# Kernel tuning notes

Hardware: AMD Instinct MI355X
Metric: run time of the kernel (lower is better)

Reference implementation:

```python
import jax, jax.numpy as jnp
import numpy as np

B, S, C = 128, 512, 64
H, D = 4, 32  # num_heads, units


def setup_inputs() -> dict:
    key = jax.random.key(0)
    ks = jax.random.split(key, 6)
    scale_in = 1.0 / np.sqrt(C)
    scale_cat = 1.0 / np.sqrt(H * D)
    return {
        "inputs": jax.random.normal(ks[0], (B, S, C), dtype=jnp.float32),
        "Wq": jax.random.normal(ks[1], (H, C, D), dtype=jnp.float32) * scale_in,
        "bq": jnp.zeros((H, D), dtype=jnp.float32),
        "Wk": jax.random.normal(ks[2], (H, C, D), dtype=jnp.float32) * scale_in,
        "bk": jnp.zeros((H, D), dtype=jnp.float32),
        "Wv": jax.random.normal(ks[3], (H, C, D), dtype=jnp.float32) * scale_in,
        "bv": jnp.zeros((H, D), dtype=jnp.float32),
        "Wo": jax.random.normal(ks[4], (H * D, D), dtype=jnp.float32) * scale_cat,
        "bo": jnp.zeros((D,), dtype=jnp.float32),
    }


def reference(inputs, Wq, bq, Wk, bk, Wv, bv, Wo, bo):
    # Batched QKV projections over all heads at once (fuses the per-head loop).
    # inputs: [B,S,C]; Wq/Wk/Wv: [H,C,D]; biases: [H,D]
    Q = jnp.einsum("bsc,hcd->bhsd", inputs, Wq) + bq[None, :, None, :]
    K = jnp.einsum("bsc,hcd->bhsd", inputs, Wk) + bk[None, :, None, :]
    V = jnp.einsum("bsc,hcd->bhsd", inputs, Wv) + bv[None, :, None, :]
    scale = 1.0 / jnp.sqrt(jnp.asarray(D, dtype=inputs.dtype))
    scores = jnp.einsum("bhsd,bhtd->bhst", Q, K) * scale  # [B,H,S,S]
    attn = jax.nn.softmax(scores, axis=-1)
    ctx = jnp.einsum("bhst,bhtd->bhsd", attn, V)  # [B,H,S,D]
    # Concatenate heads along feature dim (head 0 first, matching tf.concat order)
    concat = jnp.transpose(ctx, (0, 2, 1, 3)).reshape(inputs.shape[0], inputs.shape[1], H * D)
    return concat @ Wo + bo
```

## Files before the change

kernel.cpp:

```cpp
#include <hip/hip_runtime.h>
#include <hip/hip_bf16.h>

#define B_ 128
#define S_ 512
#define C_ 64
#define H_ 4
#define D_ 32
#define QSCALE_LOG2E 0.25505654249765306f

typedef __attribute__((ext_vector_type(8))) short bf16x8;
typedef __attribute__((ext_vector_type(8))) unsigned short u16x8;
typedef __attribute__((ext_vector_type(4))) unsigned short u16x4;
typedef __attribute__((ext_vector_type(4))) float f32x4;
typedef __attribute__((ext_vector_type(4))) unsigned int u32x4;
typedef __attribute__((ext_vector_type(2))) unsigned int u32x2;

__device__ __forceinline__ unsigned short f2bf(float f) {
    unsigned int u = __float_as_uint(f);
    u = (u + 0x7FFFu + ((u >> 16) & 1u)) >> 16;
    return (unsigned short)u;
}
__device__ __forceinline__ unsigned int pk2(float a, float b) {
    __hip_bfloat162 h = __float22bfloat162_rn(float2{a, b});
    unsigned int r;
    __builtin_memcpy(&r, &h, sizeof(r));
    return r;
}

__global__ __launch_bounds__(256) void wprep_kernel(
    const float* __restrict__ Wq, const float* __restrict__ bq,
    const float* __restrict__ Wk, const float* __restrict__ bk,
    const float* __restrict__ Wv, const float* __restrict__ bv,
    unsigned short* __restrict__ Wt, float* __restrict__ bias)
{
    const int bid = blockIdx.x, tid = threadIdx.x;
    if (bid < 96) {
        const int idx = bid * 256 + tid;
        const int m = idx >> 13, f = idx & 8191;
        const int h = f >> 11, c = (f >> 5) & 63, d = f & 31;
        const float* W = (m == 0) ? Wq : (m == 1) ? Wk : Wv;
        float v = W[f] * ((m == 0) ? QSCALE_LOG2E : 1.0f);
        Wt[(size_t)(m * 128 + h * 32 + d) * 64 + c] = f2bf(v);
    } else {
        for (int idx = tid; idx < 384; idx += 256) {
            int m = idx >> 7, o = idx & 127;
            const float* bs = (m == 0) ? bq : (m == 1) ? bk : bv;
            bias[idx] = bs[o] * ((m == 0) ? QSCALE_LOG2E : 1.0f);
        }
    }
}

__global__ __launch_bounds__(256, 4) void qkv_kernel(
    const float* __restrict__ X, const unsigned short* __restrict__ Wt,
    const float* __restrict__ bias,
    unsigned short* __restrict__ Qo, unsigned short* __restrict__ Ko,
    unsigned short* __restrict__ Vo)
{
    __shared__ unsigned int Xs[128 * 36];

    const int tid  = threadIdx.x;
    const int row0 = blockIdx.x * 128;
    const int w    = tid >> 6, lane = tid & 63;
    const int lq   = lane & 15, lg = lane >> 4;

    {
        const float4* Xg = reinterpret_cast<const float4*>(X + (size_t)row0 * C_);
        #pragma unroll
        for (int k = 0; k < 8; ++k) {
            int f4 = tid + k * 256;
            int r = f4 >> 4, c4 = f4 & 15;
            float4 x = Xg[f4];
            u32x2 p;
            p[0] = pk2(x.x, x.y);
            p[1] = pk2(x.z, x.w);
            *reinterpret_cast<u32x2*>(&Xs[r * 36 + c4 * 2]) = p;
        }
    }
    __syncthreads();

    const int b  = row0 / S_;
    const int sb = row0 % S_;

    #pragma unroll
    for (int m = 0; m < 3; ++m) {
        const unsigned short* Wtm = Wt + (size_t)(m * 128) * 64;
        const float* bm = bias + m * 128;
        unsigned short* Out = (m == 0) ? Qo : (m == 1) ? Ko : Vo;

        #pragma unroll
        for (int ni = 0; ni < 2; ++ni) {
            const int nt = 2 * w + ni;
            const int n0 = nt * 16;
            bf16x8 wf0 = *reinterpret_cast<const bf16x8*>(Wtm + (size_t)(n0 + lq) * 64 + lg * 8);
            bf16x8 wf1 = *reinterpret_cast<const bf16x8*>(Wtm + (size_t)(n0 + lq) * 64 + 32 + lg * 8);

            if (m != 2) {
                const int nrow = n0 + 4 * lg;
                const int h = nrow >> 5, d0 = nrow & 31;
                f32x4 bv4 = *reinterpret_cast<const f32x4*>(bm + nrow);
                unsigned short* obase = Out + ((size_t)(b * H_ + h) * S_ + sb) * D_ + d0;
                #pragma unroll
                for (int st = 0; st < 8; ++st) {
                    const unsigned int* xr = &Xs[(st * 16 + lq) * 36];
                    bf16x8 xf0 = *reinterpret_cast<const bf16x8*>(xr + lg * 4);
                    bf16x8 xf1 = *reinterpret_cast<const bf16x8*>(xr + 16 + lg * 4);
                    f32x4 acc;
                    acc[0] = 0.f; acc[1] = 0.f; acc[2] = 0.f; acc[3] = 0.f;
                    acc = __builtin_amdgcn_mfma_f32_16x16x32_bf16(wf0, xf0, acc, 0, 0, 0);
                    acc = __builtin_amdgcn_mfma_f32_16x16x32_bf16(wf1, xf1, acc, 0, 0, 0);
                    u32x2 cc;
                    cc[0] = pk2(acc[0] + bv4[0], acc[1] + bv4[1]);
                    cc[1] = pk2(acc[2] + bv4[2], acc[3] + bv4[3]);
                    *reinterpret_cast<u32x2*>(obase + (size_t)(st * 16 + lq) * D_) = cc;
                }
            } else {
                const int ncol = n0 + lq;
                const int h = ncol >> 5, d = ncol & 31;
                const float bsc = bm[ncol];
                unsigned short* obase = Out + ((size_t)(b * H_ + h) * S_) * D_
                                      + (size_t)d * S_ + sb + 4 * lg;
                #pragma unroll
                for (int st = 0; st < 8; ++st) {
                    const unsigned int* xr = &Xs[(st * 16 + lq) * 36];
                    bf16x8 xf0 = *reinterpret_cast<const bf16x8*>(xr + lg * 4);
                    bf16x8 xf1 = *reinterpret_cast<const bf16x8*>(xr + 16 + lg * 4);
                    f32x4 acc;
                    acc[0] = 0.f; acc[1] = 0.f; acc[2] = 0.f; acc[3] = 0.f;
                    acc = __builtin_amdgcn_mfma_f32_16x16x32_bf16(xf0, wf0, acc, 0, 0, 0);
                    acc = __builtin_amdgcn_mfma_f32_16x16x32_bf16(xf1, wf1, acc, 0, 0, 0);
                    u32x2 cc;
                    cc[0] = pk2(acc[0] + bsc, acc[1] + bsc);
                    cc[1] = pk2(acc[2] + bsc, acc[3] + bsc);
                    *reinterpret_cast<u32x2*>(obase + st * 16) = cc;
                }
            }
        }
    }
}

__global__ __launch_bounds__(1024) void attn_kernel(
    const unsigned short* __restrict__ Qb, const unsigned short* __restrict__ Kb,
    const unsigned short* __restrict__ Vtb, unsigned short* __restrict__ ctx)
{
    __shared__ unsigned short Ks[512 * 40];
    __shared__ unsigned short Vs[32 * 524];

    const int bh  = blockIdx.x;
    const int b   = bh >> 2, h = bh & 3;
    const int tid = threadIdx.x;
    const int w   = tid >> 6, lane = tid & 63;
    const int lq  = lane & 15, lg = lane >> 4;

    const unsigned short* Qp = Qb  + (size_t)bh * (S_ * D_);
    const unsigned short* Kp = Kb  + (size_t)bh * (S_ * D_);
    const unsigned short* Vp = Vtb + (size_t)bh * (S_ * D_);

    #pragma unroll
    for (int it = 0; it < 2; ++it) {
        int idx = it * 1024 + tid;
        int r = idx >> 2, q4 = idx & 3;
        u16x8 x = *reinterpret_cast<const u16x8*>(Kp + r * 32 + q4 * 8);
        *reinterpret_cast<u16x8*>(&Ks[r * 40 + q4 * 8]) = x;
    }
    #pragma unroll
    for (int it = 0; it < 2; ++it) {
        int idx = it * 1024 + tid;
        int r = idx >> 6, c = idx & 63;
        u16x8 x = *reinterpret_cast<const u16x8*>(Vp + r * 512 + c * 8);
        u16x4 lo; lo[0] = x[0]; lo[1] = x[1]; lo[2] = x[2]; lo[3] = x[3];
        u16x4 hi; hi[0] = x[4]; hi[1] = x[5]; hi[2] = x[6]; hi[3] = x[7];
        *reinterpret_cast<u16x4*>(&Vs[r * 524 + c * 8])     = lo;
        *reinterpret_cast<u16x4*>(&Vs[r * 524 + c * 8 + 4]) = hi;
    }
    __syncthreads();

    const int q0 = w * 32;

    bf16x8 qf[2];
    #pragma unroll
    for (int qi = 0; qi < 2; ++qi)
        qf[qi] = *reinterpret_cast<const bf16x8*>(
            Qp + (size_t)(q0 + qi * 16 + lq) * D_ + lg * 8);

    u32x4 onesu;
    onesu[0] = 0x3F803F80u; onesu[1] = 0x3F803F80u;
    onesu[2] = 0x3F803F80u; onesu[3] = 0x3F803F80u;
    const bf16x8 vones = __builtin_bit_cast(bf16x8, onesu);

    f32x4 acc[2][2];
    f32x4 lacc[2];
    #pragma unroll
    for (int qi = 0; qi < 2; ++qi) {
        lacc[qi][0] = 0.f; lacc[qi][1] = 0.f; lacc[qi][2] = 0.f; lacc[qi][3] = 0.f;
        #pragma unroll
        for (int dt = 0; dt < 2; ++dt) {
            acc[qi][dt][0] = 0.f; acc[qi][dt][1] = 0.f;
            acc[qi][dt][2] = 0.f; acc[qi][dt][3] = 0.f;
        }
    }

    const unsigned short* kl0 = &Ks[lq * 40 + lg * 8];
    const unsigned short* kl1 = &Ks[(16 + lq) * 40 + lg * 8];
    const unsigned short* vl0 = &Vs[lq * 524 + 4 * lg];
    const unsigned short* vl1 = &Vs[(16 + lq) * 524 + 4 * lg];

    #pragma unroll 2
    for (int tc = 0; tc < 16; ++tc) {
        const int t0 = tc * 32;
        bf16x8 k0 = *reinterpret_cast<const bf16x8*>(kl0 + t0 * 40);
        bf16x8 k1 = *reinterpret_cast<const bf16x8*>(kl1 + t0 * 40);

        u32x2 va = *reinterpret_cast<const u32x2*>(vl0 + t0);
        u32x2 vb = *reinterpret_cast<const u32x2*>(vl0 + t0 + 16);
        u32x2 vc = *reinterpret_cast<const u32x2*>(vl1 + t0);
        u32x2 vd = *reinterpret_cast<const u32x2*>(vl1 + t0 + 16);
        u32x4 v0u; v0u[0] = va[0]; v0u[1] = va[1]; v0u[2] = vb[0]; v0u[3] = vb[1];
        u32x4 v1u; v1u[0] = vc[0]; v1u[1] = vc[1]; v1u[2] = vd[0]; v1u[3] = vd[1];
        bf16x8 v0 = __builtin_bit_cast(bf16x8, v0u);
        bf16x8 v1 = __builtin_bit_cast(bf16x8, v1u);

        __builtin_amdgcn_s_setprio(1);
        #pragma unroll
        for (int qi = 0; qi < 2; ++qi) {
            f32x4 z; z[0] = 0.f; z[1] = 0.f; z[2] = 0.f; z[3] = 0.f;
            f32x4 s0 = __builtin_amdgcn_mfma_f32_16x16x32_bf16(k0, qf[qi], z, 0, 0, 0);
            f32x4 s1 = __builtin_amdgcn_mfma_f32_16x16x32_bf16(k1, qf[qi], z, 0, 0, 0);
            float pa = __builtin_amdgcn_exp2f(s0[0]);
            float pb = __builtin_amdgcn_exp2f(s0[1]);
            float pc = __builtin_amdgcn_exp2f(s0[2]);
            float pd = __builtin_amdgcn_exp2f(s0[3]);
            float pe = __builtin_amdgcn_exp2f(s1[0]);
            float pf = __builtin_amdgcn_exp2f(s1[1]);
            float pg = __builtin_amdgcn_exp2f(s1[2]);
            float ph = __builtin_amdgcn_exp2f(s1[3]);
            u32x4 pu;
            pu[0] = pk2(pa, pb);
            pu[1] = pk2(pc, pd);
            pu[2] = pk2(pe, pf);
            pu[3] = pk2(pg, ph);
            bf16x8 pfr = __builtin_bit_cast(bf16x8, pu);
            acc[qi][0] = __builtin_amdgcn_mfma_f32_16x16x32_bf16(v0, pfr, acc[qi][0], 0, 0, 0);
            acc[qi][1] = __builtin_amdgcn_mfma_f32_16x16x32_bf16(v1, pfr, acc[qi][1], 0, 0, 0);
            lacc[qi]   = __builtin_amdgcn_mfma_f32_16x16x32_bf16(vones, pfr, lacc[qi], 0, 0, 0);
        }
        __builtin_amdgcn_s_setprio(0);
    }

    #pragma unroll
    for (int qi = 0; qi < 2; ++qi) {
        const float inv = 1.0f / lacc[qi][0];
        const int qg = q0 + qi * 16 + lq;
        #pragma unroll
        for (int dt = 0; dt < 2; ++dt) {
            u32x2 c;
            c[0] = pk2(acc[qi][dt][0] * inv, acc[qi][dt][1] * inv);
            c[1] = pk2(acc[qi][dt][2] * inv, acc[qi][dt][3] * inv);
            unsigned short* cp = ctx + ((size_t)(b * S_ + qg)) * (H_ * D_)
                               + h * D_ + dt * 16 + lg * 4;
            *reinterpret_cast<u32x2*>(cp) = c;
        }
    }
}

__global__ __launch_bounds__(256) void out_kernel(
    const unsigned short* __restrict__ ctx, const float* __restrict__ Wo,
    const float* __restrict__ bo, float* __restrict__ out)
{
    __shared__ float4 Wos[128][8];
    const int tid = threadIdx.x;
    #pragma unroll
    for (int k = 0; k < 4; ++k) {
        int f4 = tid + k * 256;
        reinterpret_cast<float4*>(&Wos[0][0])[f4] =
            reinterpret_cast<const float4*>(Wo)[f4];
    }
    __syncthreads();

    const int r  = blockIdx.x * 32 + (tid >> 3);
    const int cq = tid & 7;
    const u32x4* c4 = reinterpret_cast<const u32x4*>(ctx + (size_t)r * 128);
    float4 b4 = reinterpret_cast<const float4*>(bo)[cq];
    float ax = b4.x, ay = b4.y, az = b4.z, aw = b4.w;

    #pragma unroll 4
    for (int o8 = 0; o8 < 16; ++o8) {
        u32x4 u = c4[o8];
        #pragma unroll
        for (int q = 0; q < 4; ++q) {
            float xlo = __uint_as_float(u[q] << 16);
            float xhi = __uint_as_float(u[q] & 0xFFFF0000u);
            float4 wlo = Wos[o8 * 8 + q * 2][cq];
            float4 whi = Wos[o8 * 8 + q * 2 + 1][cq];
            ax += xlo * wlo.x + xhi * whi.x;
            ay += xlo * wlo.y + xhi * whi.y;
            az += xlo * wlo.z + xhi * whi.z;
            aw += xlo * wlo.w + xhi * whi.w;
        }
    }
    reinterpret_cast<float4*>(out + (size_t)r * 32)[cq] = make_float4(ax, ay, az, aw);
}

extern "C" void kernel_launch(void* const* d_in, const int* in_sizes, int n_in,
                              void* d_out, int out_size, void* d_ws, size_t ws_size,
                              hipStream_t stream) {
    const float* X  = (const float*)d_in[0];
    const float* Wq = (const float*)d_in[1];
    const float* bq = (const float*)d_in[2];
    const float* Wk = (const float*)d_in[3];
    const float* bk = (const float*)d_in[4];
    const float* Wv = (const float*)d_in[5];
    const float* bv = (const float*)d_in[6];
    const float* Wo = (const float*)d_in[7];
    const float* bo = (const float*)d_in[8];
    float* out = (float*)d_out;

    const size_t per = (size_t)B_ * H_ * S_ * D_;
    const size_t need = 4 * per * sizeof(unsigned short) + 24576 * 2 + 384 * 4;
    if (ws_size < need) return;

    unsigned short* Qb   = (unsigned short*)d_ws;
    unsigned short* Kb   = Qb + per;
    unsigned short* Vtb  = Kb + per;
    unsigned short* ctx  = Vtb + per;
    unsigned short* Wt   = ctx + per;
    float*          bias = (float*)(Wt + 24576);

    wprep_kernel<<<97, 256, 0, stream>>>(Wq, bq, Wk, bk, Wv, bv, Wt, bias);
    qkv_kernel<<<512, 256, 0, stream>>>(X, Wt, bias, Qb, Kb, Vtb);
    attn_kernel<<<512, 1024, 0, stream>>>(Qb, Kb, Vtb, ctx);
    out_kernel<<<2048, 256, 0, stream>>>(ctx, Wo, bo, out);
}
```

Before: 68.16 us.

## Move output projection onto bf16 MFMA with pre-transposed Wo

```diff
diff --git a/kernel.cpp b/kernel.cpp
--- a/kernel.cpp
+++ b/kernel.cpp
@@ -31,7 +31,9 @@
     const float* __restrict__ Wq, const float* __restrict__ bq,
     const float* __restrict__ Wk, const float* __restrict__ bk,
     const float* __restrict__ Wv, const float* __restrict__ bv,
-    unsigned short* __restrict__ Wt, float* __restrict__ bias)
+    const float* __restrict__ Wo,
+    unsigned short* __restrict__ Wt, float* __restrict__ bias,
+    unsigned short* __restrict__ Wt2)
 {
     const int bid = blockIdx.x, tid = threadIdx.x;
     if (bid < 96) {
@@ -41,11 +43,16 @@
         const float* W = (m == 0) ? Wq : (m == 1) ? Wk : Wv;
         float v = W[f] * ((m == 0) ? QSCALE_LOG2E : 1.0f);
         Wt[(size_t)(m * 128 + h * 32 + d) * 64 + c] = f2bf(v);
-    } else {
+    } else if (bid == 96) {
         for (int idx = tid; idx < 384; idx += 256) {
             int m = idx >> 7, o = idx & 127;
             const float* bs = (m == 0) ? bq : (m == 1) ? bk : bv;
             bias[idx] = bs[o] * ((m == 0) ? QSCALE_LOG2E : 1.0f);
+        }
+    } else {
+        for (int idx = tid; idx < 4096; idx += 256) {
+            int n = idx >> 7, c = idx & 127;
+            Wt2[idx] = f2bf(Wo[c * 32 + n]);
         }
     }
 }
@@ -262,42 +269,59 @@
     }
 }
 
-__global__ __launch_bounds__(256) void out_kernel(
-    const unsigned short* __restrict__ ctx, const float* __restrict__ Wo,
+__global__ __launch_bounds__(256, 4) void out_kernel(
+    const unsigned short* __restrict__ ctx, const unsigned short* __restrict__ Wt2,
     const float* __restrict__ bo, float* __restrict__ out)
 {
-    __shared__ float4 Wos[128][8];
-    const int tid = threadIdx.x;
-    #pragma unroll
-    for (int k = 0; k < 4; ++k) {
+    __shared__ unsigned int Cs[128 * 68];
+
+    const int tid  = threadIdx.x;
+    const int row0 = blockIdx.x * 128;
+    const int w    = tid >> 6, lane = tid & 63;
+    const int lq   = lane & 15, lg = lane >> 4;
+
+    #pragma unroll
+    for (int k = 0; k < 8; ++k) {
         int f4 = tid + k * 256;
-        reinterpret_cast<float4*>(&Wos[0][0])[f4] =
-            reinterpret_cast<const float4*>(Wo)[f4];
+        int r = f4 >> 4, c4 = f4 & 15;
+        u16x8 x = *reinterpret_cast<const u16x8*>(ctx + (size_t)(row0 + r) * 128 + c4 * 8);
+        *reinterpret_cast<u16x8*>(&Cs[r * 68 + c4 * 4]) = x;
     }
     __syncthreads();
 
-    const int r  = blockIdx.x * 32 + (tid >> 3);
-    const int cq = tid & 7;
-    const u32x4* c4 = reinterpret_cast<const u32x4*>(ctx + (size_t)r * 128);
-    float4 b4 = reinterpret_cast<const float4*>(bo)[cq];
-    float ax = b4.x, ay = b4.y, az = b4.z, aw = b4.w;
-
-    #pragma unroll 4
-    for (int o8 = 0; o8 < 16; ++o8) {
-        u32x4 u = c4[o8];
-        #pragma unroll
-        for (int q = 0; q < 4; ++q) {
-            float xlo = __uint_as_float(u[q] << 16);
-            float xhi = __uint_as_float(u[q] & 0xFFFF0000u);
-            float4 wlo = Wos[o8 * 8 + q * 2][cq];
-            float4 whi = Wos[o8 * 8 + q * 2 + 1][cq];
-            ax += xlo * wlo.x + xhi * whi.x;
-            ay += xlo * wlo.y + xhi * whi.y;
-            az += xlo * wlo.z + xhi * whi.z;
-            aw += xlo * wlo.w + xhi * whi.w;
-        }
-    }
-    reinterpret_cast<float4*>(out + (size_t)r * 32)[cq] = make_float4(ax, ay, az, aw);
+    bf16x8 wf[2][4];
+    #pragma unroll
+    for (int nt = 0; nt < 2; ++nt)
+        #pragma unroll
+        for (int kk = 0; kk < 4; ++kk)
+            wf[nt][kk] = *reinterpret_cast<const bf16x8*>(
+                Wt2 + (size_t)(nt * 16 + lq) * 128 + kk * 32 + lg * 8);
+
+    const int nrow = 4 * lg;
+    f32x4 bv0, bv1;
+    #pragma unroll
+    for (int j = 0; j < 4; ++j) { bv0[j] = bo[nrow + j]; bv1[j] = bo[16 + nrow + j]; }
+
+    #pragma unroll
+    for (int i = 0; i < 2; ++i) {
+        const int st = w * 2 + i;
+        const unsigned int* xr = &Cs[(st * 16 + lq) * 68];
+        f32x4 a0, a1;
+        a0[0] = 0.f; a0[1] = 0.f; a0[2] = 0.f; a0[3] = 0.f;
+        a1[0] = 0.f; a1[1] = 0.f; a1[2] = 0.f; a1[3] = 0.f;
+        #pragma unroll
+        for (int kk = 0; kk < 4; ++kk) {
+            bf16x8 xf = *reinterpret_cast<const bf16x8*>(xr + kk * 16 + lg * 4);
+            a0 = __builtin_amdgcn_mfma_f32_16x16x32_bf16(wf[0][kk], xf, a0, 0, 0, 0);
+            a1 = __builtin_amdgcn_mfma_f32_16x16x32_bf16(wf[1][kk], xf, a1, 0, 0, 0);
+        }
+        float* op = out + (size_t)(row0 + st * 16 + lq) * 32;
+        f32x4 r0, r1;
+        #pragma unroll
+        for (int j = 0; j < 4; ++j) { r0[j] = a0[j] + bv0[j]; r1[j] = a1[j] + bv1[j]; }
+        *reinterpret_cast<f32x4*>(op + nrow)      = r0;
+        *reinterpret_cast<f32x4*>(op + 16 + nrow) = r1;
+    }
 }
 
 extern "C" void kernel_launch(void* const* d_in, const int* in_sizes, int n_in,
@@ -315,7 +339,8 @@
     float* out = (float*)d_out;
 
     const size_t per = (size_t)B_ * H_ * S_ * D_;
-    const size_t need = 4 * per * sizeof(unsigned short) + 24576 * 2 + 384 * 4;
+    const size_t need = 4 * per * sizeof(unsigned short)
+                      + 24576 * 2 + 384 * 4 + 4096 * 2;
     if (ws_size < need) return;
 
     unsigned short* Qb   = (unsigned short*)d_ws;
@@ -324,9 +349,10 @@
     unsigned short* ctx  = Vtb + per;
     unsigned short* Wt   = ctx + per;
     float*          bias = (float*)(Wt + 24576);
-
-    wprep_kernel<<<97, 256, 0, stream>>>(Wq, bq, Wk, bk, Wv, bv, Wt, bias);
+    unsigned short* Wt2  = (unsigned short*)(bias + 384);
+
+    wprep_kernel<<<98, 256, 0, stream>>>(Wq, bq, Wk, bk, Wv, bv, Wo, Wt, bias, Wt2);
     qkv_kernel<<<512, 256, 0, stream>>>(X, Wt, bias, Qb, Kb, Vtb);
     attn_kernel<<<512, 1024, 0, stream>>>(Qb, Kb, Vtb, ctx);
-    out_kernel<<<2048, 256, 0, stream>>>(ctx, Wo, bo, out);
-}
+    out_kernel<<<512, 256, 0, stream>>>(ctx, Wt2, bo, out);
+}
```

Measured after the change: 62.47 us (median of 2 runs). 8.3% less time.
